# Kernel optimization log

Measured on AMD Instinct MI355X. Metric: run time of the kernel, lower is better.

Reference implementation:

```python
import jax, jax.numpy as jnp
import numpy as np

NP, NC, E, EL = 50000, 5000, 200000, 100000
DP, DC, HID, OUT, HEADS = 1280, 256, 128, 128, 4


def setup_inputs() -> dict:
    key = jax.random.key(0)
    ks = jax.random.split(key, 40)
    p = lambda k, shp: jax.random.normal(k, shp, dtype=jnp.float32) * 0.05
    inp = {
        "x_protein": jax.random.normal(ks[0], (NP, DP), dtype=jnp.float32),
        "x_class": jax.random.normal(ks[1], (NC, DC), dtype=jnp.float32),
        "src": jax.random.randint(ks[2], (E,), 0, NP),
        "dst": jax.random.randint(ks[3], (E,), 0, NC),
        "edge_label_src": jax.random.randint(ks[4], (EL,), 0, NP),
        "edge_label_dst": jax.random.randint(ks[5], (EL,), 0, NC),
        # SAGEConv, relation protein->class (updates class nodes)
        "sage_pc_Wl": p(ks[6], (DP, HID)), "sage_pc_bl": p(ks[7], (HID,)), "sage_pc_Wr": p(ks[8], (DC, HID)),
        # SAGEConv, relation class->protein (updates protein nodes)
        "sage_cp_Wl": p(ks[9], (DC, HID)), "sage_cp_bl": p(ks[10], (HID,)), "sage_cp_Wr": p(ks[11], (DP, HID)),
        # GATConv p->c (inputs are hidden after conv1)
        "gat_pc_Wsrc": p(ks[12], (HID, HEADS * HID)), "gat_pc_Wdst": p(ks[13], (HID, HEADS * HID)),
        "gat_pc_asrc": p(ks[14], (HEADS, HID)), "gat_pc_adst": p(ks[15], (HEADS, HID)), "gat_pc_b": p(ks[16], (HID,)),
        # GATConv c->p
        "gat_cp_Wsrc": p(ks[17], (HID, HEADS * HID)), "gat_cp_Wdst": p(ks[18], (HID, HEADS * HID)),
        "gat_cp_asrc": p(ks[19], (HEADS, HID)), "gat_cp_adst": p(ks[20], (HEADS, HID)), "gat_cp_b": p(ks[21], (HID,)),
        # final per-node-type Linear (to_hetero duplicates lin per node type)
        "lin_p_W": p(ks[22], (HID, OUT)), "lin_p_b": p(ks[23], (OUT,)),
        "lin_c_W": p(ks[24], (HID, OUT)), "lin_c_b": p(ks[25], (OUT,)),
        # link predictor
        "link_W": p(ks[26], (2 * OUT, 1)), "link_b": p(ks[27], (1,)),
    }
    return inp


def _sage(x_src, x_dst, s, d, Wl, bl, Wr, n_dst):
    # PyG SAGEConv: lin_l(mean_aggr(x_src)) + lin_r(x_dst); lin_l has bias.
    agg = jax.ops.segment_sum(x_src[s], d, num_segments=n_dst)
    cnt = jax.ops.segment_sum(jnp.ones((s.shape[0], 1), x_src.dtype), d, num_segments=n_dst)
    mean = agg / jnp.maximum(cnt, 1.0)
    return mean @ Wl + bl + x_dst @ Wr


def _gat(x_src, x_dst, s, d, Ws, Wd, a_s, a_d, b, n_dst):
    # PyG GATConv bipartite, heads=HEADS, concat=False, add_self_loops=False.
    H, C = a_s.shape
    hs = (x_src @ Ws).reshape(-1, H, C)   # [Ns, H, C]
    hd = (x_dst @ Wd).reshape(-1, H, C)   # [Nd, H, C]
    als = jnp.einsum('nhc,hc->nh', hs, a_s)
    ald = jnp.einsum('nhc,hc->nh', hd, a_d)
    e = jax.nn.leaky_relu(als[s] + ald[d], 0.2)                    # [E, H]
    emax = jax.ops.segment_max(e, d, num_segments=n_dst)          # stable softmax per dst
    ee = jnp.exp(e - emax[d])
    denom = jax.ops.segment_sum(ee, d, num_segments=n_dst)
    alpha = ee / denom[d]                                          # [E, H]
    out = jax.ops.segment_sum(alpha[:, :, None] * hs[s], d, num_segments=n_dst)  # [Nd, H, C]
    return out.mean(axis=1) + b  # concat=False -> mean over heads


def reference(x_protein, x_class, src, dst, edge_label_src, edge_label_dst,
              sage_pc_Wl, sage_pc_bl, sage_pc_Wr,
              sage_cp_Wl, sage_cp_bl, sage_cp_Wr,
              gat_pc_Wsrc, gat_pc_Wdst, gat_pc_asrc, gat_pc_adst, gat_pc_b,
              gat_cp_Wsrc, gat_cp_Wdst, gat_cp_asrc, gat_cp_adst, gat_cp_b,
              lin_p_W, lin_p_b, lin_c_W, lin_c_b, link_W, link_b):
    # Layer 1: hetero SAGE (each node type has exactly one incoming relation)
    h_c = jax.nn.relu(_sage(x_protein, x_class, src, dst, sage_pc_Wl, sage_pc_bl, sage_pc_Wr, NC))
    h_p = jax.nn.relu(_sage(x_class, x_protein, dst, src, sage_cp_Wl, sage_cp_bl, sage_cp_Wr, NP))
    # Layer 2: hetero GAT
    g_c = jax.nn.relu(_gat(h_p, h_c, src, dst, gat_pc_Wsrc, gat_pc_Wdst, gat_pc_asrc, gat_pc_adst, gat_pc_b, NC))
    g_p = jax.nn.relu(_gat(h_c, h_p, dst, src, gat_cp_Wsrc, gat_cp_Wdst, gat_cp_asrc, gat_cp_adst, gat_cp_b, NP))
    # Per-type output projection
    z_p = g_p @ lin_p_W + lin_p_b
    z_c = g_c @ lin_c_W + lin_c_b
    # Link predictor: gather, concat, linear, sigmoid
    ef = jnp.concatenate([z_p[edge_label_src], z_c[edge_label_dst]], axis=-1)  # [EL, 2*OUT]
    return jax.nn.sigmoid(ef @ link_W + link_b).squeeze(-1)
```

## Files before the change

kernel.cpp:

```cpp
#include <hip/hip_runtime.h>
#include <math.h>

#define NPROT 50000
#define NCLS  5000
#define DIMP  1280
#define DIMC  256
#define SCAN_N (NCLS + NPROT)
#define KSTEPS (DIMP/32)

#define P1B  ((NPROT+127)/128)
#define C1BY ((NCLS+63)/64)
#define C1B  (4*C1BY)

typedef float4 f4;
typedef __attribute__((ext_vector_type(8))) short short8;
typedef __attribute__((ext_vector_type(4))) float f32x4;

__device__ __forceinline__ unsigned short f2bf(float f){
    unsigned u = __float_as_uint(f);
    u += 0x7FFFu + ((u >> 16) & 1u);
    return (unsigned short)(u >> 16);
}
__device__ __forceinline__ float bf2f(unsigned short b){
    return __uint_as_float(((unsigned)b) << 16);
}
__device__ __forceinline__ void gload_lds16(const void* g, void* l){
    __builtin_amdgcn_global_load_lds((const __attribute__((address_space(1))) void*)g,
                                     (__attribute__((address_space(3))) void*)l, 16, 0, 0);
}
__device__ __forceinline__ int OFFV(const int* __restrict__ offv, const int* __restrict__ part, int v){
    return offv[v] + part[v>>10];
}

__global__ __launch_bounds__(512) void mega1(const float* __restrict__ Af,
                                             const unsigned short* __restrict__ BtP,
                                             unsigned short* __restrict__ P1,
                                             const float* __restrict__ Ac,
                                             const float* __restrict__ WcatC,
                                             unsigned short* __restrict__ C1,
                                             const int* __restrict__ src, const int* __restrict__ dst,
                                             const int* __restrict__ offv, const int* __restrict__ part,
                                             int* __restrict__ cur, int* __restrict__ adj, int E){
    __shared__ __align__(16) unsigned char smem[64*1024];
    const int blk = blockIdx.x;
    const int tid = threadIdx.x;

    if(blk < P1B){
        unsigned char* As = smem;
        unsigned char* Bs = smem + 16*1024;
        const int lane = tid & 63;
        const int w    = tid >> 6;
        const int wm   = w >> 2, wn = w & 3;
        const int row0 = blk * 128;
        const int kg = lane >> 4, fr = lane & 15;

        const int ar_  = tid >> 2;
        const int acc_ = tid & 3;
        const int asrow = min(row0 + ar_, NPROT-1);
        const float* aG = Af + (size_t)asrow*DIMP + acc_*8;
        const int awoff = ar_*64 + ((acc_ ^ ((ar_>>1)&3)) << 4);

        f32x4 acc[4][4] = {};
        f4 va, vb;

        auto STAGEB = [&](int buf, int k0){
            #pragma unroll
            for(int i=0;i<2;i++){
                int c  = i*512 + tid;
                int r  = c >> 2, cc = c & 3;
                int scc = cc ^ ((r>>1) & 3);
                gload_lds16((const void*)(BtP + (size_t)r*DIMP + k0 + scc*8),
                            (void*)(Bs + buf*16384 + (i*512 + w*64 + lane)*16));
            }
        };
        auto WRITEA = [&](int buf){
            union { short8 s; unsigned short u[8]; } uu;
            uu.u[0]=f2bf(va.x); uu.u[1]=f2bf(va.y); uu.u[2]=f2bf(va.z); uu.u[3]=f2bf(va.w);
            uu.u[4]=f2bf(vb.x); uu.u[5]=f2bf(vb.y); uu.u[6]=f2bf(vb.z); uu.u[7]=f2bf(vb.w);
            *(short8*)(As + buf*8192 + awoff) = uu.s;
        };

        va = *(const f4*)(aG + 0);
        vb = *(const f4*)(aG + 4);
        STAGEB(0, 0);
        STAGEB(1, 32);
        WRITEA(0);
        va = *(const f4*)(aG + 32);
        vb = *(const f4*)(aG + 36);

        for(int t=0; t<KSTEPS; ++t){
            if(t+1 < KSTEPS) asm volatile("s_waitcnt vmcnt(4) lgkmcnt(0)" ::: "memory");
            else             asm volatile("s_waitcnt vmcnt(0) lgkmcnt(0)" ::: "memory");
            __builtin_amdgcn_sched_barrier(0);
            __builtin_amdgcn_s_barrier();
            __builtin_amdgcn_sched_barrier(0);

            if(t+1 < KSTEPS) WRITEA((t+1)&1);
            if(t+2 < KSTEPS){
                va = *(const f4*)(aG + (t+2)*32);
                vb = *(const f4*)(aG + (t+2)*32 + 4);
                STAGEB((t+2)%3, (t+2)*32);
            }

            const unsigned char* Ab = As + (t&1)*8192;
            const unsigned char* Bb = Bs + (t%3)*16384;
            short8 aF[4], bF[4];
            #pragma unroll
            for(int m=0;m<4;m++){
                int r = wm*64 + m*16 + fr;
                aF[m] = *(const short8*)(Ab + r*64 + ((kg ^ ((r>>1)&3))<<4));
            }
            #pragma unroll
            for(int n=0;n<4;n++){
                int r = wn*64 + n*16 + fr;
                bF[n] = *(const short8*)(Bb + r*64 + ((kg ^ ((r>>1)&3))<<4));
            }
            #pragma unroll
            for(int m=0;m<4;m++)
            #pragma unroll
            for(int n=0;n<4;n++)
                acc[m][n] = __builtin_amdgcn_mfma_f32_16x16x32_bf16(aF[m], bF[n], acc[m][n], 0, 0, 0);
        }

        #pragma unroll
        for(int m=0;m<4;m++)
        #pragma unroll
        for(int r=0;r<4;r++){
            int row = row0 + wm*64 + m*16 + kg*4 + r;
            if(row < NPROT){
                #pragma unroll
                for(int n=0;n<4;n++)
                    P1[(size_t)row*256 + wn*64 + n*16 + fr] = f2bf(acc[m][n][r]);
            }
        }
    } else if(blk < P1B + C1B){
        float (*As)[68] = (float(*)[68])smem;
        float (*Bs)[64] = (float(*)[64])(smem + 16*68*4);
        const int bi = blk - P1B;
        const int row0 = (bi >> 2) * 64;
        const int col0 = (bi & 3) * 64;
        const bool act = tid < 256;
        const int ty = tid >> 4;
        const int tx = tid & 15;
        const int m  = tid >> 2;
        const int kq = (tid & 3) << 2;
        const int kb = tid >> 4;
        const int c4 = (tid & 15) << 2;

        float acc[4][4];
        #pragma unroll
        for(int i=0;i<4;i++)
        #pragma unroll
            for(int j=0;j<4;j++) acc[i][j]=0.f;

        const bool arow_ok = act && (row0 + m) < NCLS;
        const float* Abase = Ac + (size_t)(row0 + min(m,255)) * DIMC + kq;
        const float* Bbase = WcatC + col0 + c4 + (size_t)kb * 256;

        for(int k0 = 0; k0 < DIMC; k0 += 16){
            if(act){
                f4 av;
                if(arow_ok) av = *(const f4*)(Abase + k0);
                else        av = make_float4(0.f,0.f,0.f,0.f);
                As[kq+0][m]=av.x; As[kq+1][m]=av.y; As[kq+2][m]=av.z; As[kq+3][m]=av.w;
                *(f4*)&Bs[kb][c4] = *(const f4*)(Bbase + (size_t)k0 * 256);
            }
            __syncthreads();
            if(act){
                #pragma unroll
                for(int kk=0;kk<16;kk++){
                    f4 a = *(const f4*)&As[kk][ty<<2];
                    f4 b = *(const f4*)&Bs[kk][tx<<2];
                    float ar[4]={a.x,a.y,a.z,a.w};
                    float br[4]={b.x,b.y,b.z,b.w};
                    #pragma unroll
                    for(int i=0;i<4;i++)
                    #pragma unroll
                        for(int j=0;j<4;j++) acc[i][j] += ar[i]*br[j];
                }
            }
            __syncthreads();
        }
        if(act){
            #pragma unroll
            for(int i=0;i<4;i++){
                int r = row0 + (ty<<2) + i;
                if(r < NCLS){
                    ushort4 v;
                    v.x=f2bf(acc[i][0]); v.y=f2bf(acc[i][1]);
                    v.z=f2bf(acc[i][2]); v.w=f2bf(acc[i][3]);
                    *(ushort4*)&C1[(size_t)r*256 + col0 + (tx<<2)] = v;
                }
            }
        }
    } else {
        int e = (blk - P1B - C1B)*512 + tid;
        if(e < E){
            int s = src[e], d = dst[e];
            int pc = atomicAdd(&cur[d],1);        adj[OFFV(offv,part,d)+pc] = s;
            int pp = atomicAdd(&cur[NCLS+s],1);   adj[OFFV(offv,part,NCLS+s)+pp] = d;
        }
    }
}

#define NPB ((NPROT+127)/128)
#define NCB ((NCLS+127)/128)
__global__ __launch_bounds__(256) void gemm_hs(const unsigned short* __restrict__ Ap,
                                               const unsigned short* __restrict__ Ac,
                                               const unsigned short* __restrict__ Btp,
                                               const unsigned short* __restrict__ Btc,
                                               const float* __restrict__ projP,
                                               const float* __restrict__ projC,
                                               unsigned short* __restrict__ Cp,
                                               unsigned short* __restrict__ Cc,
                                               float* __restrict__ attP,
                                               float* __restrict__ attC){
    const bool cls = (int)blockIdx.y >= NPB;
    const unsigned short* A  = cls ? Ac : Ap;
    const unsigned short* Bt = cls ? Btc : Btp;
    unsigned short* C = cls ? Cc : Cp;
    const int M = cls ? NCLS : NPROT;
    const int row0 = (cls ? blockIdx.y - NPB : blockIdx.y) * 128;
    const int col0 = blockIdx.x * 128;

    __shared__ __align__(16) unsigned char As[128*32*2];
    __shared__ __align__(16) unsigned char Bs[128*32*2];
    __shared__ float projS[1024];
    const int tid  = threadIdx.x;
    const int lane = tid & 63;
    const int w    = tid >> 6;
    const int wm   = w >> 1, wn = w & 1;
    const int kg = lane >> 4, fr = lane & 15;

    f32x4 acc[4][4] = {};

    for(int k0 = 0; k0 < 128; k0 += 32){
        #pragma unroll
        for(int i=0;i<2;i++){
            int c  = i*256 + w*64 + lane;
            int r  = c >> 2, cc = c & 3;
            int scc = cc ^ ((r>>1) & 3);
            int srow = min(row0 + r, M-1);
            gload_lds16((const void*)(A + (size_t)srow*128 + k0 + scc*8),
                        (void*)(As + (i*256 + w*64)*16));
        }
        #pragma unroll
        for(int i=0;i<2;i++){
            int c  = i*256 + w*64 + lane;
            int r  = c >> 2, cc = c & 3;
            int scc = cc ^ ((r>>1) & 3);
            gload_lds16((const void*)(Bt + (size_t)(col0 + r)*128 + k0 + scc*8),
                        (void*)(Bs + (i*256 + w*64)*16));
        }
        __syncthreads();

        short8 aF[4], bF[4];
        #pragma unroll
        for(int m=0;m<4;m++){
            int r = wm*64 + m*16 + fr;
            int b0 = (r*64 + kg*16) ^ (((r>>1)&3)<<4);
            aF[m] = *(const short8*)(As + b0);
        }
        #pragma unroll
        for(int n=0;n<4;n++){
            int r = wn*64 + n*16 + fr;
            int b0 = (r*64 + kg*16) ^ (((r>>1)&3)<<4);
            bF[n] = *(const short8*)(Bs + b0);
        }
        #pragma unroll
        for(int m=0;m<4;m++)
        #pragma unroll
        for(int n=0;n<4;n++)
            acc[m][n] = __builtin_amdgcn_mfma_f32_16x16x32_bf16(aF[m], bF[n], acc[m][n], 0, 0, 0);
        __syncthreads();
    }

    #pragma unroll
    for(int m=0;m<4;m++)
    #pragma unroll
    for(int r=0;r<4;r++){
        int row = row0 + wm*64 + m*16 + kg*4 + r;
        if(row < M){
            #pragma unroll
            for(int n=0;n<4;n++)
                C[(size_t)row*512 + col0 + wn*64 + n*16 + fr] = f2bf(acc[m][n][r]);
        }
    }

    if(blockIdx.x == 0){
        const float* proj = cls ? projC : projP;
        float* att = cls ? attC : attP;
        for(int i=tid;i<1024;i+=256) projS[i] = proj[i];
        __syncthreads();
        int ri = tid >> 1, cb = (tid & 1)*4;
        int row = row0 + ri;
        if(row < M){
            const unsigned short* ar = A + (size_t)row*128;
            float s0=0.f,s1=0.f,s2=0.f,s3=0.f;
            #pragma unroll
            for(int kk=0;kk<16;kk++){
                short8 a8 = *(const short8*)(ar + kk*8);
                #pragma unroll
                for(int q=0;q<8;q++){
                    float av = bf2f((unsigned short)a8[q]);
                    const float* pr = &projS[(kk*8+q)*8 + cb];
                    s0 += av*pr[0]; s1 += av*pr[1]; s2 += av*pr[2]; s3 += av*pr[3];
                }
            }
            f4 o = make_float4(s0,s1,s2,s3);
            *(f4*)&att[(size_t)row*8 + cb] = o;
        }
    }
}

__global__ void setup(const float* __restrict__ Wl_pc, const float* __restrict__ Wr_cp,
                      const float* __restrict__ Wl_cp, const float* __restrict__ Wr_pc,
                      const float* __restrict__ pcWs, const float* __restrict__ pcAs,
                      const float* __restrict__ pcWd, const float* __restrict__ pcAd,
                      const float* __restrict__ cpWs, const float* __restrict__ cpAs,
                      const float* __restrict__ cpWd, const float* __restrict__ cpAd,
                      const float* __restrict__ lpW, const float* __restrict__ lpb,
                      const float* __restrict__ lcW, const float* __restrict__ lcb,
                      const float* __restrict__ linkW,
                      const int* __restrict__ src, const int* __restrict__ dst,
                      unsigned short* __restrict__ BtP, float* __restrict__ WcatC,
                      unsigned short* __restrict__ BtSp, unsigned short* __restrict__ BtSc,
                      float* __restrict__ projP, float* __restrict__ projC,
                      float* __restrict__ w_p, float* __restrict__ w_c,
                      float* __restrict__ cpc,
                      int* __restrict__ deg, int E){
    int blk = blockIdx.x, tid = threadIdx.x;
    if(blk < 2048){
        int t = blk*256 + tid;
        if(t < 327680){
            int n = t / 1280, k = t % 1280;
            float v = (n<128) ? Wl_pc[(size_t)k*128+n] : Wr_cp[(size_t)k*128+n-128];
            BtP[t] = f2bf(v);
        } else if(t < 393216){
            int i = t - 327680; int k = i>>8, j = i&255;
            WcatC[i] = (j<128) ? Wl_cp[(size_t)k*128+j] : Wr_pc[(size_t)k*128+j-128];
        } else if(t < 458752){
            int i = t - 393216; int n = i>>7, k = i&127;
            BtSp[i] = f2bf(pcWs[(size_t)k*512+n]);
        } else {
            int i = t - 458752; int n = i>>7, k = i&127;
            BtSc[i] = f2bf(cpWs[(size_t)k*512+n]);
        }
    } else if(blk < 2056){
        int sec = (blk-2048) >> 1;
        int t = ((blk-2048) & 1)*256 + tid;
        const float *W, *a; float* proj; int colbase;
        if(sec==0){ W=pcWs; a=pcAs; proj=projP; colbase=0; }
        else if(sec==1){ W=cpWd; a=cpAd; proj=projP; colbase=4; }
        else if(sec==2){ W=pcWd; a=pcAd; proj=projC; colbase=0; }
        else { W=cpWs; a=cpAs; proj=projC; colbase=4; }
        int k = t >> 2, h = t & 3;
        const float* w = W + (size_t)k*512 + h*128;
        const float* av = a + h*128;
        float s=0.f;
        for(int c=0;c<128;c++) s += w[c]*av[c];
        proj[k*8 + colbase + h] = s;
    } else if(blk == 2056){
        if(tid < 128){
            float s=0.f;
            for(int o=0;o<128;o++) s += lpW[(size_t)tid*128+o]*linkW[o];
            w_p[tid]=s;
        } else {
            int j=tid-128;
            float s=0.f;
            for(int o=0;o<128;o++) s += lcW[(size_t)j*128+o]*linkW[128+o];
            w_c[j]=s;
        }
        if(tid==0){ float s=0.f; for(int o=0;o<128;o++) s+=lpb[o]*linkW[o];      cpc[0]=s; }
        if(tid==1){ float s=0.f; for(int o=0;o<128;o++) s+=lcb[o]*linkW[128+o];  cpc[1]=s; }
    } else {
        int e = (blk-2057)*256 + tid;
        if(e < E){
            atomicAdd(&deg[dst[e]],1);
            atomicAdd(&deg[NCLS + src[e]],1);
        }
    }
}

__global__ __launch_bounds__(1024) void scan1(const int* __restrict__ in, int* __restrict__ out,
                                              int* __restrict__ part, int n){
    __shared__ int buf[1024];
    int tid = threadIdx.x;
    int g = blockIdx.x*1024 + tid;
    int v = (g<n) ? in[g] : 0;
    buf[tid] = v;
    __syncthreads();
    for(int o=1;o<1024;o<<=1){
        int t = (tid>=o) ? buf[tid-o] : 0;
        __syncthreads();
        buf[tid] += t;
        __syncthreads();
    }
    if(g<n) out[g] = buf[tid] - v;
    if(tid==1023) part[blockIdx.x] = buf[1023];
}
__global__ __launch_bounds__(64) void scan2(int* __restrict__ part, int nb,
                                            int* __restrict__ offv, int n){
    int tid = threadIdx.x;
    int orig = (tid<nb) ? part[tid] : 0;
    int v = orig;
    #pragma unroll
    for(int o=1;o<64;o<<=1){
        int t = __shfl_up(v, o);
        if(tid>=o) v += t;
    }
    int total = __shfl(v, nb-1);
    if(tid<nb) part[tid] = v - orig;
    if(tid == (n>>10)) offv[n] = total - (v - orig);
}

__global__ __launch_bounds__(256) void sage_all(const int* __restrict__ offv, const int* __restrict__ part,
                                                const int* __restrict__ adj,
                                                const unsigned short* __restrict__ P1,
                                                const unsigned short* __restrict__ C1,
                                                const float* __restrict__ bl_pc, const float* __restrict__ bl_cp,
                                                unsigned short* __restrict__ h_c, unsigned short* __restrict__ h_p){
    int v = blockIdx.x*4 + (threadIdx.x>>6);
    int l = threadIdx.x & 63;
    if(v >= SCAN_N) return;
    int b = OFFV(offv,part,v), deg = OFFV(offv,part,v+1)-b;
    float a0=0.f, a1=0.f;
    float inv = 1.f/(float)max(deg,1);
    if(v < NCLS){
        for(int i=0;i<deg;i++){
            int s = adj[b+i];
            ushort2 w = *((const ushort2*)P1 + (size_t)s*128 + l);
            a0 += bf2f(w.x); a1 += bf2f(w.y);
        }
        ushort2 sv = *((const ushort2*)C1 + (size_t)v*128 + 64 + l);
        float h0 = fmaxf(a0*inv + bl_pc[2*l]   + bf2f(sv.x), 0.f);
        float h1 = fmaxf(a1*inv + bl_pc[2*l+1] + bf2f(sv.y), 0.f);
        ushort2 o; o.x=f2bf(h0); o.y=f2bf(h1);
        *((ushort2*)h_c + (size_t)v*64 + l) = o;
    } else {
        int m = v - NCLS;
        for(int i=0;i<deg;i++){
            int d = adj[b+i];
            ushort2 w = *((const ushort2*)C1 + (size_t)d*128 + l);
            a0 += bf2f(w.x); a1 += bf2f(w.y);
        }
        ushort2 sv = *((const ushort2*)P1 + (size_t)m*128 + 64 + l);
        float h0 = fmaxf(a0*inv + bl_cp[2*l]   + bf2f(sv.x), 0.f);
        float h1 = fmaxf(a1*inv + bl_cp[2*l+1] + bf2f(sv.y), 0.f);
        ushort2 o; o.x=f2bf(h0); o.y=f2bf(h1);
        *((ushort2*)h_p + (size_t)m*64 + l) = o;
    }
}

__global__ __launch_bounds__(128) void gat_all(const int* __restrict__ offv, const int* __restrict__ part,
                                               const int* __restrict__ adj,
                                               const float* __restrict__ attP, const float* __restrict__ attC,
                                               const unsigned short* __restrict__ hs_p,
                                               const unsigned short* __restrict__ hs_c,
                                               const float* __restrict__ gb_pc, const float* __restrict__ gb_cp,
                                               const float* __restrict__ w_c, const float* __restrict__ w_p,
                                               const float* __restrict__ cpc,
                                               float* __restrict__ u_c, float* __restrict__ u_p){
    __shared__ float ald[4];
    __shared__ int   adjS[32];
    __shared__ float eeS[32*4];
    __shared__ float den8[8];
    __shared__ f4    red4[32];

    int n = blockIdx.x;
    const bool cls = n < NCLS;
    const int node = cls ? n : n - NCLS;
    const float* attS = cls ? attP : attC;
    const float* attD = cls ? attC : attP;
    const int abase = cls ? 0 : 4;
    const unsigned short* hs = cls ? hs_p : hs_c;
    const float* gb = cls ? gb_pc : gb_cp;
    const float* wv = cls ? w_c : w_p;
    float* u = cls ? u_c : u_p;
    const int cidx = cls ? 1 : 0;

    int j = threadIdx.x;
    const int hh = j >> 5;
    const int q  = j & 31;
    int b = OFFV(offv,part,n), deg = OFFV(offv,part,n+1)-b;
    if(j < 4) ald[j] = attD[(size_t)node*8 + abase + j];

    float a0=0.f, a1=0.f, a2=0.f, a3=0.f;
    float denP = 0.f;

    for(int base=0; base<deg; base+=32){
        int cnt = min(32, deg-base);
        if(j < cnt) adjS[j] = adj[b+base+j];
        __syncthreads();
        if(j < cnt*4){
            int i = j>>2, h = j&3;
            int s = adjS[i];
            float e = attS[(size_t)s*8 + abase + h] + ald[h];
            e = e > 0.f ? e : 0.2f*e;
            float ee = __expf(e);
            eeS[j] = ee;
            denP += ee;
        }
        __syncthreads();
        for(int ii=0; ii<cnt; ii++){
            int s = adjS[ii];
            float ee = eeS[ii*4 + hh];
            ushort4 v = *(const ushort4*)(hs + (size_t)s*512 + hh*128 + q*4);
            a0 += ee*bf2f(v.x); a1 += ee*bf2f(v.y);
            a2 += ee*bf2f(v.z); a3 += ee*bf2f(v.w);
        }
        __syncthreads();
    }

    float dp = denP;
    dp += __shfl_xor(dp, 4);
    dp += __shfl_xor(dp, 8);
    dp += __shfl_xor(dp, 16);
    dp += __shfl_xor(dp, 32);
    if((j & 63) < 4) den8[(j>>6)*4 + (j&3)] = dp;
    __syncthreads();

    float den_h = den8[hh] + den8[4+hh];
    float inv = (deg > 0) ? 0.25f/den_h : 0.f;
    a0 *= inv; a1 *= inv; a2 *= inv; a3 *= inv;

    a0 += __shfl_xor(a0, 32); a1 += __shfl_xor(a1, 32);
    a2 += __shfl_xor(a2, 32); a3 += __shfl_xor(a3, 32);
    if(j >= 64 && j < 96) red4[q] = make_float4(a0,a1,a2,a3);
    __syncthreads();
    float val = 0.f;
    if(j < 32){
        f4 r = red4[q];
        float t0 = a0 + r.x, t1 = a1 + r.y, t2 = a2 + r.z, t3 = a3 + r.w;
        const float* gbq = gb + q*4;
        const float* wvq = wv + q*4;
        val = fmaxf(t0 + gbq[0], 0.f)*wvq[0]
            + fmaxf(t1 + gbq[1], 0.f)*wvq[1]
            + fmaxf(t2 + gbq[2], 0.f)*wvq[2]
            + fmaxf(t3 + gbq[3], 0.f)*wvq[3];
    }
    #pragma unroll
    for(int o=16;o;o>>=1) val += __shfl_down(val, o);
    if(j == 0) u[node] = val + cpc[cidx];
}

__global__ void link_out(const int* __restrict__ els, const int* __restrict__ eld,
                         const float* __restrict__ u_p, const float* __restrict__ u_c,
                         const float* __restrict__ linkb, float* __restrict__ out, int EL){
    int i = blockIdx.x*256 + threadIdx.x;
    if(i >= EL) return;
    float x = u_p[els[i]] + u_c[eld[i]] + linkb[0];
    out[i] = 1.f/(1.f + __expf(-x));
}

extern "C" void kernel_launch(void* const* d_in, const int* in_sizes, int n_in,
                              void* d_out, int out_size, void* d_ws, size_t ws_size,
                              hipStream_t stream){
    const float* x_p  = (const float*)d_in[0];
    const float* x_c  = (const float*)d_in[1];
    const int*   src  = (const int*)d_in[2];
    const int*   dst  = (const int*)d_in[3];
    const int*   els  = (const int*)d_in[4];
    const int*   eld  = (const int*)d_in[5];
    const float* sage_pc_Wl = (const float*)d_in[6];
    const float* sage_pc_bl = (const float*)d_in[7];
    const float* sage_pc_Wr = (const float*)d_in[8];
    const float* sage_cp_Wl = (const float*)d_in[9];
    const float* sage_cp_bl = (const float*)d_in[10];
    const float* sage_cp_Wr = (const float*)d_in[11];
    const float* gat_pc_Wsrc = (const float*)d_in[12];
    const float* gat_pc_Wdst = (const float*)d_in[13];
    const float* gat_pc_asrc = (const float*)d_in[14];
    const float* gat_pc_adst = (const float*)d_in[15];
    const float* gat_pc_b    = (const float*)d_in[16];
    const float* gat_cp_Wsrc = (const float*)d_in[17];
    const float* gat_cp_Wdst = (const float*)d_in[18];
    const float* gat_cp_asrc = (const float*)d_in[19];
    const float* gat_cp_adst = (const float*)d_in[20];
    const float* gat_cp_b    = (const float*)d_in[21];
    const float* lin_p_W = (const float*)d_in[22];
    const float* lin_p_b = (const float*)d_in[23];
    const float* lin_c_W = (const float*)d_in[24];
    const float* lin_c_b = (const float*)d_in[25];
    const float* link_W  = (const float*)d_in[26];
    const float* link_b  = (const float*)d_in[27];

    const int E  = in_sizes[2];
    const int EL = in_sizes[4];

    float* ws = (float*)d_ws;
    size_t off = 0;
    auto alloc = [&](size_t n)->float*{ float* p = ws + off; off += (n + 3) & ~(size_t)3; return p; };

    unsigned short* BtP  = (unsigned short*)alloc((size_t)256*DIMP/2);
    float* WcatC = alloc((size_t)DIMC*256);
    unsigned short* BtSp = (unsigned short*)alloc((size_t)512*128/2);
    unsigned short* BtSc = (unsigned short*)alloc((size_t)512*128/2);
    unsigned short* P1   = (unsigned short*)alloc((size_t)NPROT*256/2);
    unsigned short* C1   = (unsigned short*)alloc((size_t)NCLS*256/2);
    unsigned short* h_p  = (unsigned short*)alloc((size_t)NPROT*128/2);
    unsigned short* h_c  = (unsigned short*)alloc((size_t)NCLS*128/2);
    unsigned short* hs_p = (unsigned short*)alloc((size_t)NPROT*512/2);
    unsigned short* hs_c = (unsigned short*)alloc((size_t)NCLS*512/2);
    float* attP  = alloc((size_t)NPROT*8);
    float* attC  = alloc((size_t)NCLS*8);
    float* projP = alloc(128*8);
    float* projC = alloc(128*8);
    float* w_p   = alloc(128);
    float* w_c   = alloc(128);
    float* cpc   = alloc(4);
    int* degcur = (int*)alloc((size_t)2*SCAN_N);
    int* deg = degcur;
    int* cur = degcur + SCAN_N;
    int* offv = (int*)alloc(SCAN_N+1);
    int* part = (int*)alloc(64);
    int* adj  = (int*)alloc((size_t)2*E);
    float* u_p = alloc(NPROT);
    float* u_c = alloc(NCLS);
    if(off*4 > ws_size) return;

    hipMemsetAsync(degcur, 0, (size_t)2*SCAN_N*4, stream);

    setup<<<2057 + (E+255)/256, 256, 0, stream>>>(
        sage_pc_Wl, sage_cp_Wr, sage_cp_Wl, sage_pc_Wr,
        gat_pc_Wsrc, gat_pc_asrc, gat_pc_Wdst, gat_pc_adst,
        gat_cp_Wsrc, gat_cp_asrc, gat_cp_Wdst, gat_cp_adst,
        lin_p_W, lin_p_b, lin_c_W, lin_c_b, link_W,
        src, dst,
        BtP, WcatC, BtSp, BtSc, projP, projC, w_p, w_c, cpc, deg, E);

    const int NB = (SCAN_N + 1023)/1024;
    scan1<<<NB,1024,0,stream>>>(deg, offv, part, SCAN_N);
    scan2<<<1,64,0,stream>>>(part, NB, offv, SCAN_N);

    const int FILLB = (E+511)/512;
    mega1<<<P1B + C1B + FILLB, 512, 0, stream>>>(x_p, BtP, P1, x_c, WcatC, C1,
                                                 src, dst, offv, part, cur, adj, E);

    sage_all<<<(SCAN_N+3)/4,256,0,stream>>>(offv, part, adj, P1, C1, sage_pc_bl, sage_cp_bl, h_c, h_p);

    gemm_hs<<<dim3(4,NPB+NCB),256,0,stream>>>(h_p, h_c, BtSp, BtSc, projP, projC,
                                              hs_p, hs_c, attP, attC);

    gat_all<<<SCAN_N,128,0,stream>>>(offv, part, adj, attP, attC, hs_p, hs_c,
                                     gat_pc_b, gat_cp_b, w_c, w_p, cpc, u_c, u_p);

    link_out<<<(EL+255)/256,256,0,stream>>>(els, eld, u_p, u_c, link_b, (float*)d_out, EL);
}
```

Baseline: 318.7 us.

## Switch protein GEMM B staging to double buffer, cut LDS, unroll gather loops

The bf16 MFMA GEMM in mega1 stages B tiles with two LDS buffers instead of three, issuing each stage one step ahead and moving the wait to the end of each iteration. This drops the LDS allocation from 64KB to 48KB, which may let more blocks fit per CU. The cost is a shorter prefetch distance for B, so global-load latency may be less hidden. Separately, the neighbour-gather loops in sage_all and gat_all get unroll-4 pragmas to put more loads in flight.

```diff
diff --git a/kernel.cpp b/kernel.cpp
--- a/kernel.cpp
+++ b/kernel.cpp
@@ -41,7 +41,7 @@
                                              const int* __restrict__ src, const int* __restrict__ dst,
                                              const int* __restrict__ offv, const int* __restrict__ part,
                                              int* __restrict__ cur, int* __restrict__ adj, int E){
-    __shared__ __align__(16) unsigned char smem[64*1024];
+    __shared__ __align__(16) unsigned char smem[48*1024];
     const int blk = blockIdx.x;
     const int tid = threadIdx.x;
 
@@ -70,7 +70,7 @@
                 int r  = c >> 2, cc = c & 3;
                 int scc = cc ^ ((r>>1) & 3);
                 gload_lds16((const void*)(BtP + (size_t)r*DIMP + k0 + scc*8),
-                            (void*)(Bs + buf*16384 + (i*512 + w*64 + lane)*16));
+                            (void*)(Bs + buf*16384 + (i*512 + tid)*16));
             }
         };
         auto WRITEA = [&](int buf){
@@ -80,30 +80,31 @@
             *(short8*)(As + buf*8192 + awoff) = uu.s;
         };
 
+        STAGEB(0, 0);
         va = *(const f4*)(aG + 0);
         vb = *(const f4*)(aG + 4);
-        STAGEB(0, 0);
-        STAGEB(1, 32);
         WRITEA(0);
         va = *(const f4*)(aG + 32);
         vb = *(const f4*)(aG + 36);
+        asm volatile("s_waitcnt lgkmcnt(0)" ::: "memory");
+        __builtin_amdgcn_sched_barrier(0);
 
         for(int t=0; t<KSTEPS; ++t){
-            if(t+1 < KSTEPS) asm volatile("s_waitcnt vmcnt(4) lgkmcnt(0)" ::: "memory");
-            else             asm volatile("s_waitcnt vmcnt(0) lgkmcnt(0)" ::: "memory");
-            __builtin_amdgcn_sched_barrier(0);
             __builtin_amdgcn_s_barrier();
             __builtin_amdgcn_sched_barrier(0);
 
-            if(t+1 < KSTEPS) WRITEA((t+1)&1);
+            if(t+1 < KSTEPS){
+                WRITEA((t+1)&1);
+                STAGEB((t+1)&1, (t+1)*32);
+            }
+            __builtin_amdgcn_sched_barrier(0);
             if(t+2 < KSTEPS){
                 va = *(const f4*)(aG + (t+2)*32);
                 vb = *(const f4*)(aG + (t+2)*32 + 4);
-                STAGEB((t+2)%3, (t+2)*32);
             }
 
             const unsigned char* Ab = As + (t&1)*8192;
-            const unsigned char* Bb = Bs + (t%3)*16384;
+            const unsigned char* Bb = Bs + (t&1)*16384;
             short8 aF[4], bF[4];
             #pragma unroll
             for(int m=0;m<4;m++){
@@ -120,6 +121,10 @@
             #pragma unroll
             for(int n=0;n<4;n++)
                 acc[m][n] = __builtin_amdgcn_mfma_f32_16x16x32_bf16(aF[m], bF[n], acc[m][n], 0, 0, 0);
+
+            if(t+2 < KSTEPS)      asm volatile("s_waitcnt vmcnt(2) lgkmcnt(0)" ::: "memory");
+            else                  asm volatile("s_waitcnt vmcnt(0) lgkmcnt(0)" ::: "memory");
+            __builtin_amdgcn_sched_barrier(0);
         }
 
         #pragma unroll
@@ -134,8 +139,8 @@
             }
         }
     } else if(blk < P1B + C1B){
-        float (*As)[68] = (float(*)[68])smem;
-        float (*Bs)[64] = (float(*)[64])(smem + 16*68*4);
+        float (*As64)[68] = (float(*)[68])smem;
+        float (*Bs64)[64] = (float(*)[64])(smem + 16*68*4);
         const int bi = blk - P1B;
         const int row0 = (bi >> 2) * 64;
         const int col0 = (bi & 3) * 64;
@@ -155,22 +160,22 @@
 
         const bool arow_ok = act && (row0 + m) < NCLS;
         const float* Abase = Ac + (size_t)(row0 + min(m,255)) * DIMC + kq;
-        const float* Bbase = WcatC + col0 + c4 + (size_t)kb * 256;
+        const float* Bbase = WcatC + col0 + c4 + (size_t)min(kb,15) * 256;
 
         for(int k0 = 0; k0 < DIMC; k0 += 16){
             if(act){
                 f4 av;
                 if(arow_ok) av = *(const f4*)(Abase + k0);
                 else        av = make_float4(0.f,0.f,0.f,0.f);
-                As[kq+0][m]=av.x; As[kq+1][m]=av.y; As[kq+2][m]=av.z; As[kq+3][m]=av.w;
-                *(f4*)&Bs[kb][c4] = *(const f4*)(Bbase + (size_t)k0 * 256);
+                As64[kq+0][m]=av.x; As64[kq+1][m]=av.y; As64[kq+2][m]=av.z; As64[kq+3][m]=av.w;
+                *(f4*)&Bs64[kb][c4] = *(const f4*)(Bbase + (size_t)k0 * 256);
             }
             __syncthreads();
             if(act){
                 #pragma unroll
                 for(int kk=0;kk<16;kk++){
-                    f4 a = *(const f4*)&As[kk][ty<<2];
-                    f4 b = *(const f4*)&Bs[kk][tx<<2];
+                    f4 a = *(const f4*)&As64[kk][ty<<2];
+                    f4 b = *(const f4*)&Bs64[kk][tx<<2];
                     float ar[4]={a.x,a.y,a.z,a.w};
                     float br[4]={b.x,b.y,b.z,b.w};
                     #pragma unroll
@@ -427,6 +432,7 @@
     float a0=0.f, a1=0.f;
     float inv = 1.f/(float)max(deg,1);
     if(v < NCLS){
+        #pragma unroll 4
         for(int i=0;i<deg;i++){
             int s = adj[b+i];
             ushort2 w = *((const ushort2*)P1 + (size_t)s*128 + l);
@@ -439,6 +445,7 @@
         *((ushort2*)h_c + (size_t)v*64 + l) = o;
     } else {
         int m = v - NCLS;
+        #pragma unroll 4
         for(int i=0;i<deg;i++){
             int d = adj[b+i];
             ushort2 w = *((const ushort2*)C1 + (size_t)d*128 + l);
@@ -502,6 +509,7 @@
             denP += ee;
         }
         __syncthreads();
+        #pragma unroll 4
         for(int ii=0; ii<cnt; ii++){
             int s = adjS[ii];
             float ee = eeS[ii*4 + hh];
```

Measured after the change: 315.7 us. No clear change (-0.9%).
